# Kernel tuning notes

Hardware: AMD Instinct MI355X
Metric: run time of the kernel (lower is better)

Reference implementation:

```python
import jax, jax.numpy as jnp
import numpy as np

B, TE, H = 32, 8192, 128  # batch, encoder seq len, hidden

def setup_inputs() -> dict:
    key = jax.random.key(0)
    k1, k2, k3, k4, k5 = jax.random.split(key, 5)
    return {
        "encoder_out_seq": jax.random.normal(k1, (B, TE, H), dtype=jnp.float32),
        "decoder_out_seq": jax.random.normal(k2, (B, 1, H), dtype=jnp.float32),
        "W_a": jax.random.normal(k3, (H, H), dtype=jnp.float32) * 0.05,
        "U_a": jax.random.normal(k4, (H, H), dtype=jnp.float32) * 0.05,
        "V_a": jax.random.normal(k5, (H, 1), dtype=jnp.float32) * 0.05,
    }

def reference(encoder_out_seq, decoder_out_seq, W_a, U_a, V_a):
    # W_a . s : [B, TE, H]
    Ws = jnp.einsum('beh,hk->bek', encoder_out_seq, W_a)
    # U_a . h : [B, 1, H] (single decoder step, broadcasts over TE)
    Uh = jnp.einsum('bdh,hk->bdk', decoder_out_seq, U_a)
    # energy scores: tanh then project to scalar -> [B, TE]
    scores = jnp.einsum('bek,ko->be', jnp.tanh(Ws + Uh), V_a)
    e_i = jax.nn.softmax(scores, axis=-1)            # [B, TE]
    c_i = jnp.einsum('be,beh->bh', e_i, encoder_out_seq)  # context [B, H]
    return (e_i, c_i)
```

## Files before the change

kernel.cpp:

```cpp
#include <hip/hip_runtime.h>
#include <hip/hip_bf16.h>

#define B_  32
#define TE_ 8192
#define H_  128
#define M_  (B_ * TE_)

typedef __bf16 bf16x8 __attribute__((ext_vector_type(8)));
typedef float  f32x4  __attribute__((ext_vector_type(4)));

#define WS_UH    0
#define WS_WP    4096
#define WS_LACC  (4096 + 8192)
#define WS_CACC  (WS_LACC + 32)

__device__ __forceinline__ float tanh_fast(float x) {
  x = fminf(10.f, fmaxf(-10.f, x));
  float e = __expf(2.f * x);
  return (e - 1.f) * __builtin_amdgcn_rcpf(e + 1.f);
}

__global__ __launch_bounds__(256) void prep_kernel(
    const float* __restrict__ dec, const float* __restrict__ U,
    const float* __restrict__ W, float* __restrict__ ws) {
  int tid = blockIdx.x * 256 + threadIdx.x;
  int b = tid >> 7, k = tid & 127;
  const float* dp = dec + b * H_;
  float s = 0.f;
  #pragma unroll 8
  for (int h = 0; h < H_; ++h) s += dp[h] * U[h * H_ + k];
  ws[WS_UH + tid] = s;

  ws[WS_CACC + tid] = 0.f;
  if (tid < 32) ws[WS_LACC + tid] = 0.f;

  __bf16* Wp = (__bf16*)(ws + WS_WP);
  for (int i = tid; i < H_ * H_; i += 4096) {
    int j = i & 7;
    int lane = (i >> 3) & 63;
    int f = i >> 9;
    int sK = f & 3, nt = f >> 2;
    int kk = sK * 32 + (lane >> 4) * 8 + j;
    int nn = nt * 16 + (lane & 15);
    Wp[i] = (__bf16)W[kk * H_ + nn];
  }
}

__global__ __launch_bounds__(256, 4) void fused_kernel(
    const float* __restrict__ enc, const float* __restrict__ ws_in,
    const float* __restrict__ V, float* __restrict__ wout,
    float* __restrict__ ws) {
  __shared__ uint4 ldsW[2048];
  __shared__ float pcbuf[4][H_];
  __shared__ float lsum[4];

  int t = threadIdx.x;
  const uint4* wsrc = (const uint4*)(ws_in + WS_WP);
  for (int i = t; i < 2048; i += 256) ldsW[i] = wsrc[i];

  int wave = t >> 6, lane = t & 63;
  int l15 = lane & 15, quad = lane >> 4;
  int blockRow = blockIdx.x << 8;
  int b = blockRow >> 13;

  float uh[8], vl[8];
  #pragma unroll
  for (int nt = 0; nt < 8; ++nt) {
    uh[nt] = ws_in[WS_UH + b * H_ + nt * 16 + l15];
    vl[nt] = V[nt * 16 + l15];
  }
  __syncthreads();

  float cacc[32];
  #pragma unroll
  for (int k = 0; k < 32; ++k) cacc[k] = 0.f;
  float Lpart = 0.f;

  const float4* rp0 = (const float4*)(enc + (size_t)(blockRow + (wave << 4) + l15) * H_) + quad * 2;
  const int stripStride = 4 * 16 * (H_ / 4);

  float4 buf[8];
  #pragma unroll
  for (int s = 0; s < 4; ++s) {
    buf[2 * s]     = rp0[s * 8];
    buf[2 * s + 1] = rp0[s * 8 + 1];
  }

  #pragma unroll
  for (int it = 0; it < 4; ++it) {
    bf16x8 af[4];
    #pragma unroll
    for (int s = 0; s < 4; ++s) {
      float4 lo = buf[2 * s], hi = buf[2 * s + 1];
      bf16x8 a;
      a[0] = (__bf16)lo.x; a[1] = (__bf16)lo.y; a[2] = (__bf16)lo.z; a[3] = (__bf16)lo.w;
      a[4] = (__bf16)hi.x; a[5] = (__bf16)hi.y; a[6] = (__bf16)hi.z; a[7] = (__bf16)hi.w;
      af[s] = a;
    }
    if (it < 3) {
      const float4* rp = rp0 + (it + 1) * stripStride;
      #pragma unroll
      for (int s = 0; s < 4; ++s) {
        buf[2 * s]     = rp[s * 8];
        buf[2 * s + 1] = rp[s * 8 + 1];
      }
    }

    float p0 = 0.f, p1 = 0.f, p2 = 0.f, p3 = 0.f;
    #pragma unroll
    for (int nt = 0; nt < 8; ++nt) {
      f32x4 acc = {0.f, 0.f, 0.f, 0.f};
      #pragma unroll
      for (int s = 0; s < 4; ++s) {
        union { uint4 u; bf16x8 v; } bw;
        bw.u = ldsW[(nt * 4 + s) * 64 + lane];
        acc = __builtin_amdgcn_mfma_f32_16x16x32_bf16(af[s], bw.v, acc, 0, 0, 0);
      }
      float u = uh[nt], vv = vl[nt];
      p0 += tanh_fast(acc[0] + u) * vv;
      p1 += tanh_fast(acc[1] + u) * vv;
      p2 += tanh_fast(acc[2] + u) * vv;
      p3 += tanh_fast(acc[3] + u) * vv;
    }
    #pragma unroll
    for (int m = 1; m < 16; m <<= 1) {
      p0 += __shfl_xor(p0, m, 64);
      p1 += __shfl_xor(p1, m, 64);
      p2 += __shfl_xor(p2, m, 64);
      p3 += __shfl_xor(p3, m, 64);
    }
    float w0 = __expf(p0), w1 = __expf(p1), w2 = __expf(p2), w3 = __expf(p3);
    int rowBase = blockRow + ((it * 4 + wave) << 4);
    if (l15 < 4) {
      float v = (l15 == 0) ? w0 : (l15 == 1) ? w1 : (l15 == 2) ? w2 : w3;
      wout[rowBase + quad * 4 + l15] = v;
    }
    Lpart += w0 + w1 + w2 + w3;

    int srcLane = (l15 >> 2) << 4;
    float q0 = __shfl(w0, srcLane, 64);
    float q1 = __shfl(w1, srcLane, 64);
    float q2 = __shfl(w2, srcLane, 64);
    float q3 = __shfl(w3, srcLane, 64);
    int r = l15 & 3;
    float wrow = (r == 0) ? q0 : (r == 1) ? q1 : (r == 2) ? q2 : q3;

    #pragma unroll
    for (int s = 0; s < 4; ++s) {
      #pragma unroll
      for (int j = 0; j < 8; ++j)
        cacc[s * 8 + j] += wrow * (float)af[s][j];
    }
  }

  #pragma unroll
  for (int m = 1; m < 16; m <<= 1) {
    #pragma unroll
    for (int k = 0; k < 32; ++k)
      cacc[k] += __shfl_xor(cacc[k], m, 64);
  }
  if (l15 == 0) {
    #pragma unroll
    for (int s = 0; s < 4; ++s)
      #pragma unroll
      for (int j = 0; j < 8; ++j)
        pcbuf[wave][s * 32 + quad * 8 + j] = cacc[s * 8 + j];
  }
  Lpart += __shfl_xor(Lpart, 16, 64);
  Lpart += __shfl_xor(Lpart, 32, 64);
  if (lane == 0) lsum[wave] = Lpart;
  __syncthreads();

  if (t < H_) {
    float s = pcbuf[0][t] + pcbuf[1][t] + pcbuf[2][t] + pcbuf[3][t];
    atomicAdd(&ws[WS_CACC + b * H_ + t], s);
  }
  if (t == 0)
    atomicAdd(&ws[WS_LACC + b], lsum[0] + lsum[1] + lsum[2] + lsum[3]);
}

__global__ __launch_bounds__(256) void finalize_kernel(
    float* __restrict__ e, float* __restrict__ c, const float* __restrict__ ws) {
  int t = threadIdx.x;
  if (blockIdx.x < 256) {
    int i4 = blockIdx.x * 256 + t;
    int b = i4 >> 11;
    float inv = 1.f / ws[WS_LACC + b];
    float4 v = ((float4*)e)[i4];
    v.x *= inv; v.y *= inv; v.z *= inv; v.w *= inv;
    ((float4*)e)[i4] = v;
  } else {
    #pragma unroll
    for (int k = 0; k < 16; ++k) {
      int i = k * 256 + t;
      int b = i >> 7;
      c[i] = ws[WS_CACC + i] / ws[WS_LACC + b];
    }
  }
}

extern "C" void kernel_launch(void* const* d_in, const int* in_sizes, int n_in,
                              void* d_out, int out_size, void* d_ws, size_t ws_size,
                              hipStream_t stream) {
  const float* enc = (const float*)d_in[0];
  const float* dec = (const float*)d_in[1];
  const float* Wa  = (const float*)d_in[2];
  const float* Ua  = (const float*)d_in[3];
  const float* Va  = (const float*)d_in[4];

  float* out   = (float*)d_out;
  float* e_out = out;
  float* c_out = out + B_ * TE_;
  float* ws    = (float*)d_ws;

  prep_kernel<<<16, 256, 0, stream>>>(dec, Ua, Wa, ws);
  fused_kernel<<<M_ / 256, 256, 0, stream>>>(enc, ws, Va, e_out, ws);
  finalize_kernel<<<257, 256, 0, stream>>>(e_out, c_out, ws);
}
```

Before: 220.8 us.

## Swap MFMA operands so each lane owns a row score; use nontemporal loads

Swaps the A/B operands of the bf16 MFMA so the accumulator is transposed. Each lane then holds hidden-dimension outputs for its own row, so the energy reduction needs only two cross-quad shuffles and the per-row shuffle broadcast of weights disappears. U·h and V move into LDS and are read as float4, and the partial-context buffer reuses the W LDS region. Encoder loads become nontemporal to avoid polluting the cache. This trades extra LDS reads and one added barrier for fewer shuffles and selects.

Measured after the change: 210.7 us. -4.6%, faster.

```diff
diff --git a/kernel.cpp b/kernel.cpp
--- a/kernel.cpp
+++ b/kernel.cpp
@@ -40,7 +40,7 @@
     int lane = (i >> 3) & 63;
     int f = i >> 9;
     int sK = f & 3, nt = f >> 2;
-    int kk = sK * 32 + (lane >> 4) * 8 + j;
+    int kk = sK * 32 + ((lane >> 4) & 3) * 8 + j;
     int nn = nt * 16 + (lane & 15);
     Wp[i] = (__bf16)W[kk * H_ + nn];
   }
@@ -51,39 +51,35 @@
     const float* __restrict__ V, float* __restrict__ wout,
     float* __restrict__ ws) {
   __shared__ uint4 ldsW[2048];
-  __shared__ float pcbuf[4][H_];
+  __shared__ float ldsUV[256];
   __shared__ float lsum[4];
 
   int t = threadIdx.x;
+  int blockRow = blockIdx.x << 8;
+  int b = blockRow >> 13;
+
   const uint4* wsrc = (const uint4*)(ws_in + WS_WP);
   for (int i = t; i < 2048; i += 256) ldsW[i] = wsrc[i];
+  if (t < 128) ldsUV[t] = ws_in[WS_UH + b * H_ + t];
+  else ldsUV[t] = V[t - 128];
+  __syncthreads();
 
   int wave = t >> 6, lane = t & 63;
   int l15 = lane & 15, quad = lane >> 4;
-  int blockRow = blockIdx.x << 8;
-  int b = blockRow >> 13;
-
-  float uh[8], vl[8];
-  #pragma unroll
-  for (int nt = 0; nt < 8; ++nt) {
-    uh[nt] = ws_in[WS_UH + b * H_ + nt * 16 + l15];
-    vl[nt] = V[nt * 16 + l15];
-  }
-  __syncthreads();
 
   float cacc[32];
   #pragma unroll
   for (int k = 0; k < 32; ++k) cacc[k] = 0.f;
   float Lpart = 0.f;
 
-  const float4* rp0 = (const float4*)(enc + (size_t)(blockRow + (wave << 4) + l15) * H_) + quad * 2;
+  const f32x4* rp0 = (const f32x4*)(enc + (size_t)(blockRow + (wave << 4) + l15) * H_) + quad * 2;
   const int stripStride = 4 * 16 * (H_ / 4);
 
-  float4 buf[8];
+  f32x4 buf[8];
   #pragma unroll
   for (int s = 0; s < 4; ++s) {
-    buf[2 * s]     = rp0[s * 8];
-    buf[2 * s + 1] = rp0[s * 8 + 1];
+    buf[2 * s]     = __builtin_nontemporal_load(rp0 + s * 8);
+    buf[2 * s + 1] = __builtin_nontemporal_load(rp0 + s * 8 + 1);
   }
 
   #pragma unroll
@@ -91,22 +87,22 @@
     bf16x8 af[4];
     #pragma unroll
     for (int s = 0; s < 4; ++s) {
-      float4 lo = buf[2 * s], hi = buf[2 * s + 1];
+      f32x4 lo = buf[2 * s], hi = buf[2 * s + 1];
       bf16x8 a;
-      a[0] = (__bf16)lo.x; a[1] = (__bf16)lo.y; a[2] = (__bf16)lo.z; a[3] = (__bf16)lo.w;
-      a[4] = (__bf16)hi.x; a[5] = (__bf16)hi.y; a[6] = (__bf16)hi.z; a[7] = (__bf16)hi.w;
+      a[0] = (__bf16)lo[0]; a[1] = (__bf16)lo[1]; a[2] = (__bf16)lo[2]; a[3] = (__bf16)lo[3];
+      a[4] = (__bf16)hi[0]; a[5] = (__bf16)hi[1]; a[6] = (__bf16)hi[2]; a[7] = (__bf16)hi[3];
       af[s] = a;
     }
     if (it < 3) {
-      const float4* rp = rp0 + (it + 1) * stripStride;
+      const f32x4* rp = rp0 + (it + 1) * stripStride;
       #pragma unroll
       for (int s = 0; s < 4; ++s) {
-        buf[2 * s]     = rp[s * 8];
-        buf[2 * s + 1] = rp[s * 8 + 1];
+        buf[2 * s]     = __builtin_nontemporal_load(rp + s * 8);
+        buf[2 * s + 1] = __builtin_nontemporal_load(rp + s * 8 + 1);
       }
     }
 
-    float p0 = 0.f, p1 = 0.f, p2 = 0.f, p3 = 0.f;
+    float p = 0.f;
     #pragma unroll
     for (int nt = 0; nt < 8; ++nt) {
       f32x4 acc = {0.f, 0.f, 0.f, 0.f};
@@ -114,43 +110,28 @@
       for (int s = 0; s < 4; ++s) {
         union { uint4 u; bf16x8 v; } bw;
         bw.u = ldsW[(nt * 4 + s) * 64 + lane];
-        acc = __builtin_amdgcn_mfma_f32_16x16x32_bf16(af[s], bw.v, acc, 0, 0, 0);
+        acc = __builtin_amdgcn_mfma_f32_16x16x32_bf16(bw.v, af[s], acc, 0, 0, 0);
       }
-      float u = uh[nt], vv = vl[nt];
-      p0 += tanh_fast(acc[0] + u) * vv;
-      p1 += tanh_fast(acc[1] + u) * vv;
-      p2 += tanh_fast(acc[2] + u) * vv;
-      p3 += tanh_fast(acc[3] + u) * vv;
-    }
-    #pragma unroll
-    for (int m = 1; m < 16; m <<= 1) {
-      p0 += __shfl_xor(p0, m, 64);
-      p1 += __shfl_xor(p1, m, 64);
-      p2 += __shfl_xor(p2, m, 64);
-      p3 += __shfl_xor(p3, m, 64);
-    }
-    float w0 = __expf(p0), w1 = __expf(p1), w2 = __expf(p2), w3 = __expf(p3);
+      float4 u4 = ((const float4*)ldsUV)[nt * 4 + quad];
+      float4 v4 = ((const float4*)(ldsUV + 128))[nt * 4 + quad];
+      p += tanh_fast(acc[0] + u4.x) * v4.x;
+      p += tanh_fast(acc[1] + u4.y) * v4.y;
+      p += tanh_fast(acc[2] + u4.z) * v4.z;
+      p += tanh_fast(acc[3] + u4.w) * v4.w;
+    }
+    p += __shfl_xor(p, 16, 64);
+    p += __shfl_xor(p, 32, 64);
+    float w = __expf(p);
+
     int rowBase = blockRow + ((it * 4 + wave) << 4);
-    if (l15 < 4) {
-      float v = (l15 == 0) ? w0 : (l15 == 1) ? w1 : (l15 == 2) ? w2 : w3;
-      wout[rowBase + quad * 4 + l15] = v;
-    }
-    Lpart += w0 + w1 + w2 + w3;
-
-    int srcLane = (l15 >> 2) << 4;
-    float q0 = __shfl(w0, srcLane, 64);
-    float q1 = __shfl(w1, srcLane, 64);
-    float q2 = __shfl(w2, srcLane, 64);
-    float q3 = __shfl(w3, srcLane, 64);
-    int r = l15 & 3;
-    float wrow = (r == 0) ? q0 : (r == 1) ? q1 : (r == 2) ? q2 : q3;
-
-    #pragma unroll
-    for (int s = 0; s < 4; ++s) {
+    if (quad == 0) wout[rowBase + l15] = w;
+    Lpart += w;
+
+    #pragma unroll
+    for (int s = 0; s < 4; ++s)
       #pragma unroll
       for (int j = 0; j < 8; ++j)
-        cacc[s * 8 + j] += wrow * (float)af[s][j];
-    }
+        cacc[s * 8 + j] += w * (float)af[s][j];
   }
 
   #pragma unroll
@@ -159,20 +140,25 @@
     for (int k = 0; k < 32; ++k)
       cacc[k] += __shfl_xor(cacc[k], m, 64);
   }
+  Lpart += __shfl_xor(Lpart, 1, 64);
+  Lpart += __shfl_xor(Lpart, 2, 64);
+  Lpart += __shfl_xor(Lpart, 4, 64);
+  Lpart += __shfl_xor(Lpart, 8, 64);
+
+  __syncthreads();
+  float* pcbuf = (float*)ldsW;
   if (l15 == 0) {
     #pragma unroll
     for (int s = 0; s < 4; ++s)
       #pragma unroll
       for (int j = 0; j < 8; ++j)
-        pcbuf[wave][s * 32 + quad * 8 + j] = cacc[s * 8 + j];
-  }
-  Lpart += __shfl_xor(Lpart, 16, 64);
-  Lpart += __shfl_xor(Lpart, 32, 64);
+        pcbuf[wave * H_ + s * 32 + quad * 8 + j] = cacc[s * 8 + j];
+  }
   if (lane == 0) lsum[wave] = Lpart;
   __syncthreads();
 
   if (t < H_) {
-    float s = pcbuf[0][t] + pcbuf[1][t] + pcbuf[2][t] + pcbuf[3][t];
+    float s = pcbuf[0 * H_ + t] + pcbuf[1 * H_ + t] + pcbuf[2 * H_ + t] + pcbuf[3 * H_ + t];
     atomicAdd(&ws[WS_CACC + b * H_ + t], s);
   }
   if (t == 0)
```
